# Optimization experiments

Measured on AMD Instinct MI355X. Metric: run time of the kernel, lower is better.

Reference implementation:

```python
import jax, jax.numpy as jnp
import numpy as np

M = 2          # interp_dim
D = 4          # interp_degree
MESH_LOWER = np.array([0.0, 0.0], dtype=np.float32)
MESH_UPPER = np.array([1.0, 1.0], dtype=np.float32)
MESH_SIZE = np.array([64, 64], dtype=np.int32)   # coe grid = mesh_size*D+1 = [257, 257]


def _lagrange_basis(t):
    """t: [N, M] local coordinate in [0, D]; returns bases [N, M, D+1].
    L_j(t) = prod_{k != j} (t - k) / (j - k)."""
    ks = jnp.arange(D + 1, dtype=t.dtype)
    tk = t[..., None] - ks                       # [N, M, D+1]
    bs = []
    for j in range(D + 1):                       # small fixed loop over D+1=5 bases
        num = jnp.ones(t.shape, t.dtype)
        denom = 1.0
        for k in range(D + 1):
            if k != j:
                num = num * tk[..., k]
                denom *= float(j - k)
        bs.append(num / denom)
    return jnp.stack(bs, axis=-1)                # [N, M, D+1]


def setup_inputs() -> dict:
    key = jax.random.key(0)
    k1, k2 = jax.random.split(key)
    inputs = jax.random.uniform(k1, (2048, 2048, M), dtype=jnp.float32)  # points in [0,1)^2
    grid = tuple(int(s) * D + 1 for s in MESH_SIZE)                      # (257, 257)
    interp_coe = jax.random.normal(k2, grid, dtype=jnp.float32)
    return {"inputs": inputs, "interp_coe": interp_coe}


def reference(inputs, interp_coe):
    size = inputs.shape
    x = inputs.reshape(-1, M)                                   # [N, M]
    lower = jnp.asarray(MESH_LOWER, x.dtype)
    upper = jnp.asarray(MESH_UPPER, x.dtype)
    msize = jnp.asarray(MESH_SIZE.astype(np.float32), x.dtype)
    u = (x - lower) / (upper - lower) * msize                   # grid coordinates
    cell = jnp.clip(jnp.floor(u), 0.0, msize - 1.0)             # [N, M] element index
    t = (u - cell) * D                                          # local coord in [0, D]
    basis = _lagrange_basis(t)                                  # [N, M, D+1]
    base = cell.astype(jnp.int32) * D                           # [N, M] global node base index
    offs = jnp.arange(D + 1, dtype=jnp.int32)
    i0 = base[:, 0, None] + offs                                # [N, D+1]
    i1 = base[:, 1, None] + offs                                # [N, D+1]
    coe = interp_coe[i0[:, :, None], i1[:, None, :]]            # [N, D+1, D+1] gathered cell coes
    out = jnp.einsum('nij,ni,nj->n', coe, basis[:, 0], basis[:, 1])
    return out.reshape(size[:-1])
```

## Files before the change

kernel.cpp:

```cpp
#include <hip/hip_runtime.h>

#define NGRID 257
#define LDS_PITCH 260
#define TABLE_ELEMS (NGRID * NGRID)
#define LDS_BYTES (LDS_PITCH * NGRID * 2)

typedef _Float16 half4_t __attribute__((ext_vector_type(4)));

__device__ __forceinline__ void lag_basis(float t, float b[5]) {
    float f0 = t;
    float f1 = t - 1.0f;
    float f2 = t - 2.0f;
    float f3 = t - 3.0f;
    float f4 = t - 4.0f;
    float p01 = f0 * f1;
    float p12 = f1 * f2;
    float p23 = f2 * f3;
    float p34 = f3 * f4;
    b[0] = p12 * p34 * (1.0f / 24.0f);
    b[1] = f0 * f2 * p34 * (-1.0f / 6.0f);
    b[2] = p01 * p34 * (1.0f / 4.0f);
    b[3] = p01 * f2 * f4 * (-1.0f / 6.0f);
    b[4] = p01 * p23 * (1.0f / 24.0f);
}

__device__ __forceinline__ float eval_pt(const _Float16* __restrict__ lds,
                                         float x0, float x1) {
    float u0 = x0 * 64.0f;
    float u1 = x1 * 64.0f;
    float c0 = fminf(fmaxf(floorf(u0), 0.0f), 63.0f);
    float c1 = fminf(fmaxf(floorf(u1), 0.0f), 63.0f);
    float t0 = (u0 - c0) * 4.0f;
    float t1 = (u1 - c1) * 4.0f;
    float b0[5], b1[5];
    lag_basis(t0, b0);
    lag_basis(t1, b1);
    int off = ((int)c0 * 4) * LDS_PITCH + ((int)c1 * 4);
    float acc = 0.0f;
#pragma unroll
    for (int i = 0; i < 5; ++i) {
        const _Float16* rowp = lds + off + i * LDS_PITCH;
        half4_t h4 = *(const half4_t*)rowp;
        float e4 = (float)rowp[4];
        float rd = (float)h4[0] * b1[0];
        rd = fmaf((float)h4[1], b1[1], rd);
        rd = fmaf((float)h4[2], b1[2], rd);
        rd = fmaf((float)h4[3], b1[3], rd);
        rd = fmaf(e4, b1[4], rd);
        acc = fmaf(b0[i], rd, acc);
    }
    return acc;
}

__launch_bounds__(1024, 4)
__global__ void lagrange_kernel(const float* __restrict__ inputs,
                                const float* __restrict__ coe,
                                float* __restrict__ out,
                                int npairs) {
    extern __shared__ _Float16 lds[];
    for (int e = threadIdx.x; e < TABLE_ELEMS; e += blockDim.x) {
        int r = e / NGRID;
        int c = e - r * NGRID;
        lds[r * LDS_PITCH + c] = (_Float16)coe[e];
    }
    __syncthreads();

    const float4* __restrict__ in4 = (const float4*)inputs;
    float2* __restrict__ out2 = (float2*)out;
    int stride = gridDim.x * blockDim.x;
    for (int p = blockIdx.x * blockDim.x + threadIdx.x; p < npairs; p += stride) {
        float4 v = in4[p];
        float2 r;
        r.x = eval_pt(lds, v.x, v.y);
        r.y = eval_pt(lds, v.z, v.w);
        out2[p] = r;
    }
}

extern "C" void kernel_launch(void* const* d_in, const int* in_sizes, int n_in,
                              void* d_out, int out_size, void* d_ws, size_t ws_size,
                              hipStream_t stream) {
    const float* inputs = (const float*)d_in[0];
    const float* coe    = (const float*)d_in[1];
    float* out = (float*)d_out;
    int npts = out_size;
    int npairs = npts >> 1;

    (void)hipFuncSetAttribute((const void*)lagrange_kernel,
                              hipFuncAttributeMaxDynamicSharedMemorySize,
                              LDS_BYTES);

    dim3 grid(256), block(1024);
    hipLaunchKernelGGL(lagrange_kernel, grid, block, LDS_BYTES, stream,
                       inputs, coe, out, npairs);
}
```

Before: 101.8 us.

## Vectorize LDS table fill and prefetch all per-thread inputs before evaluation

The coefficient table fill now reads four floats at a time with a packed unaligned struct and writes half4 vectors into LDS, instead of one element per thread per step with a division. The grid-stride loop becomes a fixed 8-iteration unrolled loop that issues all global input loads up front, then evaluates. Both points' LDS rows are loaded together before the arithmetic to expose more memory-level parallelism. The min-blocks launch bound is dropped. Prefetching eight float4 values raises register pressure, and the fixed ITERS count only covers inputs up to GRID*BLOCK*ITERS pairs.

```diff
diff --git a/kernel.cpp b/kernel.cpp
--- a/kernel.cpp
+++ b/kernel.cpp
@@ -2,10 +2,14 @@
 
 #define NGRID 257
 #define LDS_PITCH 260
-#define TABLE_ELEMS (NGRID * NGRID)
 #define LDS_BYTES (LDS_PITCH * NGRID * 2)
+#define BLOCK 1024
+#define GRID 256
+#define ITERS 8
 
 typedef _Float16 half4_t __attribute__((ext_vector_type(4)));
+
+struct __attribute__((packed, aligned(4))) f4u { float x, y, z, w; };
 
 __device__ __forceinline__ void lag_basis(float t, float b[5]) {
     float f0 = t;
@@ -24,56 +28,89 @@
     b[4] = p01 * p23 * (1.0f / 24.0f);
 }
 
-__device__ __forceinline__ float eval_pt(const _Float16* __restrict__ lds,
-                                         float x0, float x1) {
-    float u0 = x0 * 64.0f;
-    float u1 = x1 * 64.0f;
-    float c0 = fminf(fmaxf(floorf(u0), 0.0f), 63.0f);
-    float c1 = fminf(fmaxf(floorf(u1), 0.0f), 63.0f);
-    float t0 = (u0 - c0) * 4.0f;
-    float t1 = (u1 - c1) * 4.0f;
-    float b0[5], b1[5];
-    lag_basis(t0, b0);
-    lag_basis(t1, b1);
-    int off = ((int)c0 * 4) * LDS_PITCH + ((int)c1 * 4);
-    float acc = 0.0f;
+__device__ __forceinline__ float2 eval_pair(const _Float16* __restrict__ lds,
+                                            float4 v) {
+    float uA0 = v.x * 64.0f, uA1 = v.y * 64.0f;
+    float uB0 = v.z * 64.0f, uB1 = v.w * 64.0f;
+    float cA0 = fminf(fmaxf(floorf(uA0), 0.0f), 63.0f);
+    float cA1 = fminf(fmaxf(floorf(uA1), 0.0f), 63.0f);
+    float cB0 = fminf(fmaxf(floorf(uB0), 0.0f), 63.0f);
+    float cB1 = fminf(fmaxf(floorf(uB1), 0.0f), 63.0f);
+    float bA0[5], bA1[5], bB0[5], bB1[5];
+    lag_basis((uA0 - cA0) * 4.0f, bA0);
+    lag_basis((uA1 - cA1) * 4.0f, bA1);
+    lag_basis((uB0 - cB0) * 4.0f, bB0);
+    lag_basis((uB1 - cB1) * 4.0f, bB1);
+    int offA = ((int)cA0 * 4) * LDS_PITCH + ((int)cA1 * 4);
+    int offB = ((int)cB0 * 4) * LDS_PITCH + ((int)cB1 * 4);
+
+    half4_t hA[5], hB[5];
+    _Float16 eA[5], eB[5];
 #pragma unroll
     for (int i = 0; i < 5; ++i) {
-        const _Float16* rowp = lds + off + i * LDS_PITCH;
-        half4_t h4 = *(const half4_t*)rowp;
-        float e4 = (float)rowp[4];
-        float rd = (float)h4[0] * b1[0];
-        rd = fmaf((float)h4[1], b1[1], rd);
-        rd = fmaf((float)h4[2], b1[2], rd);
-        rd = fmaf((float)h4[3], b1[3], rd);
-        rd = fmaf(e4, b1[4], rd);
-        acc = fmaf(b0[i], rd, acc);
+        const _Float16* rA = lds + offA + i * LDS_PITCH;
+        const _Float16* rB = lds + offB + i * LDS_PITCH;
+        hA[i] = *(const half4_t*)rA;
+        hB[i] = *(const half4_t*)rB;
+        eA[i] = rA[4];
+        eB[i] = rB[4];
     }
-    return acc;
+
+    float accA = 0.0f, accB = 0.0f;
+#pragma unroll
+    for (int i = 0; i < 5; ++i) {
+        float rdA = (float)hA[i][0] * bA1[0];
+        rdA = fmaf((float)hA[i][1], bA1[1], rdA);
+        rdA = fmaf((float)hA[i][2], bA1[2], rdA);
+        rdA = fmaf((float)hA[i][3], bA1[3], rdA);
+        rdA = fmaf((float)eA[i], bA1[4], rdA);
+        accA = fmaf(bA0[i], rdA, accA);
+        float rdB = (float)hB[i][0] * bB1[0];
+        rdB = fmaf((float)hB[i][1], bB1[1], rdB);
+        rdB = fmaf((float)hB[i][2], bB1[2], rdB);
+        rdB = fmaf((float)hB[i][3], bB1[3], rdB);
+        rdB = fmaf((float)eB[i], bB1[4], rdB);
+        accB = fmaf(bB0[i], rdB, accB);
+    }
+    return make_float2(accA, accB);
 }
 
-__launch_bounds__(1024, 4)
+__launch_bounds__(BLOCK)
 __global__ void lagrange_kernel(const float* __restrict__ inputs,
                                 const float* __restrict__ coe,
                                 float* __restrict__ out,
                                 int npairs) {
     extern __shared__ _Float16 lds[];
-    for (int e = threadIdx.x; e < TABLE_ELEMS; e += blockDim.x) {
-        int r = e / NGRID;
-        int c = e - r * NGRID;
-        lds[r * LDS_PITCH + c] = (_Float16)coe[e];
+
+    for (int g = threadIdx.x; g < NGRID * 65; g += BLOCK) {
+        int r = g / 65;
+        int c4 = (g - r * 65) * 4;
+        if (c4 < 256) {
+            f4u q = *(const f4u*)(coe + r * NGRID + c4);
+            half4_t h = { (_Float16)q.x, (_Float16)q.y,
+                          (_Float16)q.z, (_Float16)q.w };
+            *(half4_t*)(lds + r * LDS_PITCH + c4) = h;
+        } else {
+            lds[r * LDS_PITCH + 256] = (_Float16)coe[r * NGRID + 256];
+        }
     }
     __syncthreads();
 
     const float4* __restrict__ in4 = (const float4*)inputs;
     float2* __restrict__ out2 = (float2*)out;
-    int stride = gridDim.x * blockDim.x;
-    for (int p = blockIdx.x * blockDim.x + threadIdx.x; p < npairs; p += stride) {
-        float4 v = in4[p];
-        float2 r;
-        r.x = eval_pt(lds, v.x, v.y);
-        r.y = eval_pt(lds, v.z, v.w);
-        out2[p] = r;
+    const int tid = blockIdx.x * BLOCK + threadIdx.x;
+    const int stride = GRID * BLOCK;
+
+    float4 v[ITERS];
+#pragma unroll
+    for (int k = 0; k < ITERS; ++k) {
+        int p = tid + k * stride;
+        if (p < npairs) v[k] = in4[p];
+    }
+#pragma unroll
+    for (int k = 0; k < ITERS; ++k) {
+        int p = tid + k * stride;
+        if (p < npairs) out2[p] = eval_pair(lds, v[k]);
     }
 }
 
@@ -83,14 +120,13 @@
     const float* inputs = (const float*)d_in[0];
     const float* coe    = (const float*)d_in[1];
     float* out = (float*)d_out;
-    int npts = out_size;
-    int npairs = npts >> 1;
+    int npairs = out_size >> 1;
 
     (void)hipFuncSetAttribute((const void*)lagrange_kernel,
                               hipFuncAttributeMaxDynamicSharedMemorySize,
                               LDS_BYTES);
 
-    dim3 grid(256), block(1024);
+    dim3 grid(GRID), block(BLOCK);
     hipLaunchKernelGGL(lagrange_kernel, grid, block, LDS_BYTES, stream,
                        inputs, coe, out, npairs);
 }
```

After: 100.4 us. About the same (-1.4%).
